# Optimization experiments

Hardware: AMD Instinct MI355X
Metric: run time of the kernel (lower is better)

Reference implementation:

```python
import jax, jax.numpy as jnp
import numpy as np

ACT_BITS = 8
NUM_HEADS = 6


def weight_quant(w):
    # BitNet b1.58 absmean ternary quantization with straight-through estimator
    scale = 1.0 / jnp.maximum(jnp.mean(jnp.abs(w)), 1e-5)
    wq = jnp.clip(jnp.round(w * scale), -1.0, 1.0) / scale
    return w + jax.lax.stop_gradient(wq - w)


def act_quant(x, bits=ACT_BITS):
    # per-token absmax quantization to `bits` bits, STE
    qb = float(2 ** (bits - 1))
    scale = qb / jnp.maximum(jnp.max(jnp.abs(x), axis=-1, keepdims=True), 1e-5)
    xq = jnp.clip(jnp.round(x * scale), -qb, qb - 1.0) / scale
    return x + jax.lax.stop_gradient(xq - x)


def bitlinear(x, w, b):
    return jnp.einsum('bnc,oc->bno', act_quant(x), weight_quant(w)) + b


def setup_inputs() -> dict:
    key = jax.random.key(0)
    ks = jax.random.split(key, 5)
    B, N, C = 8, 2048, 384
    return {
        'x': jax.random.normal(ks[0], (B, N, C), dtype=jnp.float32),
        'qkv_w': jax.random.normal(ks[1], (3 * C, C), dtype=jnp.float32) * 0.02,
        'qkv_b': jax.random.normal(ks[2], (3 * C,), dtype=jnp.float32) * 0.02,
        'proj_w': jax.random.normal(ks[3], (C, C), dtype=jnp.float32) * 0.02,
        'proj_b': jax.random.normal(ks[4], (C,), dtype=jnp.float32) * 0.02,
    }


def reference(x, qkv_w, qkv_b, proj_w, proj_b):
    B, N, C = x.shape
    H = NUM_HEADS
    D = C // H
    scale = D ** -0.5
    qkv = bitlinear(x, qkv_w, qkv_b)            # [B, N, 3C]
    q, k, v = jnp.split(qkv, 3, axis=-1)
    # [B, H, N, D]
    q = q.reshape(B, N, H, D).transpose(0, 2, 1, 3)
    k = k.reshape(B, N, H, D).transpose(0, 2, 1, 3)
    v = v.reshape(B, N, H, D).transpose(0, 2, 1, 3)
    # full [B, H, N, N] scores in float32, as in the original
    attn = jnp.einsum('bhnd,bhmd->bhnm', q.astype(jnp.float32), k.astype(jnp.float32)) * scale
    attn = jax.nn.softmax(attn, axis=-1).astype(q.dtype)
    out = jnp.einsum('bhnm,bhmd->bhnd', attn, v)
    out = out.transpose(0, 2, 1, 3).reshape(B, N, C)
    return bitlinear(out, proj_w, proj_b)
```

## Files before the change

### kernel.cpp

```cpp
#include <hip/hip_runtime.h>
#include <hip/hip_bf16.h>

typedef short  s16x8  __attribute__((ext_vector_type(8)));
typedef int    i32x4  __attribute__((ext_vector_type(4)));
typedef float  f32x16 __attribute__((ext_vector_type(16)));
typedef unsigned int u32x4 __attribute__((ext_vector_type(4)));
using u32 = unsigned int;
using u16 = unsigned short;
using as3u = __attribute__((address_space(3))) unsigned int;
using as1u = __attribute__((address_space(1))) unsigned int;

#define FINF __builtin_inff()

constexpr int B_  = 8;
constexpr int N_  = 2048;
constexpr int C_  = 384;
constexpr int H_  = 6;
constexpr int D_  = 64;
constexpr int BN_ = B_ * N_;
constexpr int O3_ = 3 * C_;
constexpr int NW1 = O3_ * C_;
constexpr int NW2 = C_ * C_;
constexpr int BH_ = B_ * H_;
constexpr int SPL = 2;

__device__ __forceinline__ u16 f2bf(float f) {
    union { float f; u32 u; } v; v.f = f;
    u32 r = v.u + 0x7FFFu + ((v.u >> 16) & 1u);
    return (u16)(r >> 16);
}
__device__ __forceinline__ float exp2a(float x) {
    float r; asm("v_exp_f32 %0, %1" : "=v"(r) : "v"(x)); return r;
}
__device__ __forceinline__ u32 cvtpk(float lo, float hi) {
    u32 r; asm("v_cvt_pk_bf16_f32 %0, %1, %2" : "=v"(r) : "v"(lo), "v"(hi)); return r;
}
__device__ __forceinline__ void plswap(u32& a, u32& b) {
    asm("v_permlane32_swap_b32 %0, %1" : "+v"(a), "+v"(b));
}
__device__ __forceinline__ float max3f(float a, float b, float c) {
    float r; asm("v_max3_f32 %0, %1, %2, %3" : "=v"(r) : "v"(a), "v"(b), "v"(c)); return r;
}
__device__ __forceinline__ u32 pack4i8(float a, float b, float c, float d) {
    int ia = (int)a, ib = (int)b, ic = (int)c, id = (int)d;
    return (u32)(ia & 255) | ((u32)(ib & 255) << 8) | ((u32)(ic & 255) << 16) | ((u32)(id & 255) << 24);
}

__global__ void k_wstats(const float* __restrict__ w1, const float* __restrict__ w2,
                         double* __restrict__ partial) {
    double s1 = 0.0, s2 = 0.0;
    int t = blockIdx.x * 256 + threadIdx.x;
    const int stride = 256 * 256;
    for (int i = t; i < NW1; i += stride) s1 += (double)fabsf(w1[i]);
    for (int i = t; i < NW2; i += stride) s2 += (double)fabsf(w2[i]);
#pragma unroll
    for (int m = 1; m < 64; m <<= 1) { s1 += __shfl_xor(s1, m, 64); s2 += __shfl_xor(s2, m, 64); }
    __shared__ double r1[4], r2[4];
    int wid = threadIdx.x >> 6;
    if ((threadIdx.x & 63) == 0) { r1[wid] = s1; r2[wid] = s2; }
    __syncthreads();
    if (threadIdx.x == 0) {
        partial[2 * blockIdx.x]     = r1[0] + r1[1] + r1[2] + r1[3];
        partial[2 * blockIdx.x + 1] = r2[0] + r2[1] + r2[2] + r2[3];
    }
}

__global__ void k_wfinal(const double* __restrict__ partial, float* __restrict__ scales) {
    int t = threadIdx.x;
    double s1 = partial[2 * t], s2 = partial[2 * t + 1];
#pragma unroll
    for (int m = 1; m < 64; m <<= 1) { s1 += __shfl_xor(s1, m, 64); s2 += __shfl_xor(s2, m, 64); }
    __shared__ double r1[4], r2[4];
    if ((t & 63) == 0) { r1[t >> 6] = s1; r2[t >> 6] = s2; }
    __syncthreads();
    if (t == 0) {
        float m1 = (float)((r1[0] + r1[1] + r1[2] + r1[3]) / (double)NW1);
        float m2 = (float)((r2[0] + r2[1] + r2[2] + r2[3]) / (double)NW2);
        float sc1 = 1.f / fmaxf(m1, 1e-5f);
        float sc2 = 1.f / fmaxf(m2, 1e-5f);
        scales[0] = sc1; scales[1] = 1.f / sc1;
        scales[2] = sc2; scales[3] = 1.f / sc2;
    }
}

__global__ void k_wquant(const float* __restrict__ w1, const float* __restrict__ w2,
                         const float* __restrict__ scales,
                         char* __restrict__ o1, char* __restrict__ o2) {
    float sc1 = scales[0], sc2 = scales[2];
    int t = blockIdx.x * blockDim.x + threadIdx.x;
    int stride = gridDim.x * blockDim.x;
    for (int i = t; i < NW1; i += stride)
        o1[i] = (char)(int)fminf(fmaxf(rintf(w1[i] * sc1), -1.f), 1.f);
    for (int i = t; i < NW2; i += stride)
        o2[i] = (char)(int)fminf(fmaxf(rintf(w2[i] * sc2), -1.f), 1.f);
}

__global__ __launch_bounds__(128) void k_aquant(const float* __restrict__ in,
                                                char* __restrict__ outq,
                                                float* __restrict__ rs) {
    int row = blockIdx.x;
    const float* xr = in + (size_t)row * C_;
    int t = threadIdx.x;
    float4 v = make_float4(0.f, 0.f, 0.f, 0.f);
    if (t < 96) v = ((const float4*)xr)[t];
    float mx = fmaxf(fmaxf(fabsf(v.x), fabsf(v.y)), fmaxf(fabsf(v.z), fabsf(v.w)));
#pragma unroll
    for (int m = 1; m < 64; m <<= 1) mx = fmaxf(mx, __shfl_xor(mx, m, 64));
    __shared__ float red[2];
    if ((t & 63) == 0) red[t >> 6] = mx;
    __syncthreads();
    mx = fmaxf(red[0], red[1]);
    float scale = 128.f / fmaxf(mx, 1e-5f);
    if (t == 0) rs[row] = 1.f / scale;
    if (t < 96) {
        float a = fminf(fmaxf(rintf(v.x * scale), -128.f), 127.f);
        float b = fminf(fmaxf(rintf(v.y * scale), -128.f), 127.f);
        float c = fminf(fmaxf(rintf(v.z * scale), -128.f), 127.f);
        float d = fminf(fmaxf(rintf(v.w * scale), -128.f), 127.f);
        ((u32*)(outq + (size_t)row * C_))[t] = pack4i8(a, b, c, d);
    }
}

template <int MODE>
__global__ __launch_bounds__(256) void k_gemm(const char* __restrict__ A, const char* __restrict__ W,
                                              const float* __restrict__ rs, const float* __restrict__ scales,
                                              const float* __restrict__ bias,
                                              u16* __restrict__ qg, u16* __restrict__ kg, u16* __restrict__ vtg,
                                              float* __restrict__ fout) {
    constexpr int K = C_;
    __shared__ char As[128 * 128];
    __shared__ char Bs[128 * 128];
    int m0 = blockIdx.x * 128, n0 = blockIdx.y * 128;
    int tid = threadIdx.x, lane = tid & 63, wid = tid >> 6;
    int wm = wid >> 1, wn = wid & 1;

    i32x4 acc[4][4];
#pragma unroll
    for (int a = 0; a < 4; ++a)
#pragma unroll
        for (int b = 0; b < 4; ++b)
#pragma unroll
            for (int r = 0; r < 4; ++r) acc[a][b][r] = 0;

    for (int k0 = 0; k0 < K; k0 += 128) {
#pragma unroll
        for (int t = 0; t < 4; ++t) {
            int P = t * 256 + wid * 64 + lane;
            int row = P >> 3, c8 = (P & 7) ^ (row & 7);
            const char* srcA = A + (size_t)(m0 + row) * K + k0 + c8 * 16;
            const char* srcB = W + (size_t)(n0 + row) * K + k0 + c8 * 16;
            __builtin_amdgcn_global_load_lds((const as1u*)srcA, (as3u*)(As + (size_t)(t * 256 + wid * 64) * 16), 16, 0, 0);
            __builtin_amdgcn_global_load_lds((const as1u*)srcB, (as3u*)(Bs + (size_t)(t * 256 + wid * 64) * 16), 16, 0, 0);
        }
        __syncthreads();
#pragma unroll
        for (int kk = 0; kk < 2; ++kk) {
            i32x4 ar[4], br[4];
#pragma unroll
            for (int f = 0; f < 4; ++f) {
                int rowA = wm * 64 + f * 16 + (lane & 15);
                int rowB = wn * 64 + f * 16 + (lane & 15);
                int cc = kk * 4 + (lane >> 4);
                ar[f] = *(const i32x4*)(&As[(size_t)(rowA * 8 + (cc ^ (rowA & 7))) * 16]);
                br[f] = *(const i32x4*)(&Bs[(size_t)(rowB * 8 + (cc ^ (rowB & 7))) * 16]);
            }
#pragma unroll
            for (int fr = 0; fr < 4; ++fr)
#pragma unroll
                for (int fc = 0; fc < 4; ++fc)
                    acc[fr][fc] = __builtin_amdgcn_mfma_i32_16x16x64_i8(ar[fr], br[fc], acc[fr][fc], 0, 0, 0);
        }
        __syncthreads();
    }

    float rsw = scales[MODE == 0 ? 1 : 3];
    int colg = lane & 15, rowb = (lane >> 4) * 4;
#pragma unroll
    for (int fr = 0; fr < 4; ++fr) {
#pragma unroll
        for (int r = 0; r < 4; ++r) {
            int m = m0 + wm * 64 + fr * 16 + rowb + r;
            float rsm = rs[m] * rsw;
#pragma unroll
            for (int fc = 0; fc < 4; ++fc) {
                int o = n0 + wn * 64 + fc * 16 + colg;
                float val = (float)acc[fr][fc][r] * rsm + bias[o];
                if (MODE == 0) {
                    int b = m >> 11, n = m & 2047;
                    if (o < C_) {
                        int hh = o >> 6, d = o & 63;
                        qg[(size_t)(b * H_ + hh) * (N_ * D_) + n * 64 + d] = f2bf(val * (0.125f * 1.44269504088896f));
                    } else if (o < 2 * C_) {
                        int oo = o - C_; int hh = oo >> 6, d = oo & 63;
                        kg[(size_t)(b * H_ + hh) * (N_ * D_) + n * 64 + d] = f2bf(val);
                    } else {
                        int oo = o - 2 * C_; int hh = oo >> 6, d = oo & 63;
                        vtg[(size_t)(b * H_ + hh) * (N_ * D_) + (size_t)d * N_ + n] = f2bf(val);
                    }
                } else {
                    fout[(size_t)m * C_ + o] = val;
                }
            }
        }
    }
}

__global__ __launch_bounds__(256, 4) void k_flash(const u16* __restrict__ qg, const u16* __restrict__ kg,
                                                  const u16* __restrict__ vtg,
                                                  float* __restrict__ pod, float* __restrict__ pml) {
    int i = blockIdx.x;
    int bh = (i & 7) * 6 + ((i >> 3) % 6);
    int x  = (i >> 3) / 6;
    int qt = x & 15;
    int split = x >> 4;
    int tid = threadIdx.x;
    int lane = tid & 63;
    int wid = tid >> 6;
    int h = lane >> 5;
    int ql = lane & 31;
    const u16* Qb = qg + (size_t)bh * (N_ * D_);
    const u16* Kb = kg + (size_t)bh * (N_ * D_);
    const u16* Vb = vtg + (size_t)bh * (N_ * D_);
    int q0 = qt * 128 + wid * 32;
    int kv_beg = split * (N_ / SPL);
    constexpr int NT = (N_ / SPL) / 64;

    __shared__ u16 Ks[2][64 * 64];
    __shared__ u16 Vs[2][64 * 64];

    s16x8 qf[4];
#pragma unroll
    for (int cs = 0; cs < 4; ++cs)
        qf[cs] = *(const s16x8*)(Qb + (size_t)(q0 + ql) * 64 + cs * 16 + h * 8);

    f32x16 od[2];
#pragma unroll
    for (int a = 0; a < 2; ++a)
#pragma unroll
        for (int r = 0; r < 16; ++r) od[a][r] = 0.f;

    float mrun = -FINF;
    float lrun = 0.f;

    auto STAGE = [&](int buf, int t0) {
        int kv0 = kv_beg + t0 * 64;
#pragma unroll
        for (int ii = 0; ii < 2; ++ii) {
            int P = (wid * 2 + ii) * 64 + lane;
            int row = P >> 3, c = (P & 7) ^ (row & 7);
            const u16* srcK = Kb + (size_t)(kv0 + row) * 64 + c * 8;
            __builtin_amdgcn_global_load_lds((const as1u*)srcK,
                (as3u*)(&Ks[buf][(size_t)(wid * 2 + ii) * 64 * 8]), 16, 0, 0);
            const u16* srcV = Vb + (size_t)row * N_ + kv0 + c * 8;
            __builtin_amdgcn_global_load_lds((const as1u*)srcV,
                (as3u*)(&Vs[buf][(size_t)(wid * 2 + ii) * 64 * 8]), 16, 0, 0);
        }
    };

    auto COMPUTE = [&](int buf) {
        f32x16 sA, sB;
#pragma unroll
        for (int r = 0; r < 16; ++r) { sA[r] = 0.f; sB[r] = 0.f; }
        __builtin_amdgcn_s_setprio(1);
#pragma unroll
        for (int cs = 0; cs < 4; ++cs) {
            int slot = (cs * 2 + h) ^ (ql & 7);
            s16x8 kf0 = *(const s16x8*)(&Ks[buf][(size_t)(ql * 8 + slot) * 8]);
            s16x8 kf1 = *(const s16x8*)(&Ks[buf][(size_t)((32 + ql) * 8 + slot) * 8]);
            sA = __builtin_amdgcn_mfma_f32_32x32x16_bf16(kf0, qf[cs], sA, 0, 0, 0);
            sB = __builtin_amdgcn_mfma_f32_32x32x16_bf16(kf1, qf[cs], sB, 0, 0, 0);
        }
        __builtin_amdgcn_s_setprio(0);

        float g0 = max3f(sA[0], sA[1], sA[2]),    g1 = max3f(sA[3], sA[4], sA[5]);
        float g2 = max3f(sA[6], sA[7], sA[8]),    g3 = max3f(sA[9], sA[10], sA[11]);
        float g4 = max3f(sA[12], sA[13], sA[14]), g5 = max3f(sA[15], sB[0], sB[1]);
        float g6 = max3f(sB[2], sB[3], sB[4]),    g7 = max3f(sB[5], sB[6], sB[7]);
        float g8 = max3f(sB[8], sB[9], sB[10]),   g9 = max3f(sB[11], sB[12], sB[13]);
        float g10 = fmaxf(sB[14], sB[15]);
        float h0 = max3f(g0, g1, g2), h1 = max3f(g3, g4, g5), h2 = max3f(g6, g7, g8);
        float mx = fmaxf(max3f(h0, h1, h2), fmaxf(g9, g10));
        mx = fmaxf(mx, __shfl_xor(mx, 32, 64));
        if (!__all(mx <= mrun + 8.f)) {
            float mnew = fmaxf(mrun, mx);
            float fsc = exp2a(mrun - mnew);
            lrun *= fsc;
#pragma unroll
            for (int r = 0; r < 16; ++r) { od[0][r] *= fsc; od[1][r] *= fsc; }
            mrun = mnew;
        }
        float m = mrun;
        float ps0 = 0.f, ps1 = 0.f, ps2 = 0.f, ps3 = 0.f;
#pragma unroll
        for (int r = 0; r < 16; r += 4) {
            float a0 = exp2a(sA[r] - m);     float a1 = exp2a(sA[r + 1] - m);
            float a2 = exp2a(sA[r + 2] - m); float a3 = exp2a(sA[r + 3] - m);
            float b0 = exp2a(sB[r] - m);     float b1 = exp2a(sB[r + 1] - m);
            float b2 = exp2a(sB[r + 2] - m); float b3 = exp2a(sB[r + 3] - m);
            sA[r] = a0; sA[r + 1] = a1; sA[r + 2] = a2; sA[r + 3] = a3;
            sB[r] = b0; sB[r + 1] = b1; sB[r + 2] = b2; sB[r + 3] = b3;
            ps0 += a0 + b0; ps1 += a1 + b1; ps2 += a2 + b2; ps3 += a3 + b3;
        }
        lrun += (ps0 + ps1) + (ps2 + ps3);

#pragma unroll
        for (int sl = 0; sl < 4; ++sl) {
            const int bse = (sl & 1) * 8;
            float p0, p1, p2, p3, p4, p5, p6, p7;
            if (sl < 2) {
                p0 = sA[bse + 0]; p1 = sA[bse + 1]; p2 = sA[bse + 2]; p3 = sA[bse + 3];
                p4 = sA[bse + 4]; p5 = sA[bse + 5]; p6 = sA[bse + 6]; p7 = sA[bse + 7];
            } else {
                p0 = sB[bse + 0]; p1 = sB[bse + 1]; p2 = sB[bse + 2]; p3 = sB[bse + 3];
                p4 = sB[bse + 4]; p5 = sB[bse + 5]; p6 = sB[bse + 6]; p7 = sB[bse + 7];
            }
            u32 A0 = cvtpk(p0, p1);
            u32 A1 = cvtpk(p2, p3);
            u32 B0 = cvtpk(p4, p5);
            u32 B1 = cvtpk(p6, p7);
            plswap(A0, B0);
            plswap(A1, B1);
            u32x4 pw; pw[0] = A0; pw[1] = A1; pw[2] = B0; pw[3] = B1;
            s16x8 pf = __builtin_bit_cast(s16x8, pw);
            __builtin_amdgcn_s_setprio(1);
#pragma unroll
            for (int db = 0; db < 2; ++db) {
                int vrow = db * 32 + ql;
                int slot = (sl * 2 + h) ^ (vrow & 7);
                s16x8 vf = *(const s16x8*)(&Vs[buf][(size_t)(vrow * 8 + slot) * 8]);
                od[db] = __builtin_amdgcn_mfma_f32_32x32x16_bf16(vf, pf, od[db], 0, 0, 0);
            }
            __builtin_amdgcn_s_setprio(0);
        }
    };

    STAGE(0, 0);
    for (int t = 0; t < NT; ++t) {
        if (t + 1 < NT) {
            STAGE((t + 1) & 1, t + 1);
            asm volatile("s_waitcnt vmcnt(4)" ::: "memory");
        } else {
            asm volatile("s_waitcnt vmcnt(0)" ::: "memory");
        }
        __builtin_amdgcn_s_barrier();
        __builtin_amdgcn_sched_barrier(0);
        COMPUTE(t & 1);
        __builtin_amdgcn_sched_barrier(0);
        __builtin_amdgcn_s_barrier();
    }

    {
        float ltot = lrun + __shfl_xor(lrun, 32, 64);
        int q = q0 + ql;
        float* op = pod + ((size_t)(split * BH_ + bh) * N_ + q) * 64;
#pragma unroll
        for (int db = 0; db < 2; ++db)
#pragma unroll
            for (int r = 0; r < 16; ++r) {
                int d = db * 32 + (r & 3) + 8 * (r >> 2) + 4 * h;
                op[d] = od[db][r];
            }
        if (h == 0) {
            float* mlp = pml + ((size_t)(split * BH_ + bh) * N_ + q) * 2;
            mlp[0] = mrun; mlp[1] = ltot;
        }
    }
}

__global__ __launch_bounds__(128) void k_caq(const float* __restrict__ pod,
                                             const float* __restrict__ pml,
                                             char* __restrict__ outq,
                                             float* __restrict__ rs) {
    int row = blockIdx.x;
    int b = row >> 11, q = row & (N_ - 1);
    int t = threadIdx.x;
    float4 o = make_float4(0.f, 0.f, 0.f, 0.f);
    if (t < 96) {
        int head = t >> 4, d4 = t & 15;
        int bh = b * H_ + head;
        const float2* ml = (const float2*)pml;
        float2 ml0 = ml[(size_t)bh * N_ + q];
        float2 ml1 = ml[(size_t)(BH_ + bh) * N_ + q];
        float m = fmaxf(ml0.x, ml1.x);
        float w0 = exp2a(ml0.x - m), w1 = exp2a(ml1.x - m);
        float inv = 1.f / (w0 * ml0.y + w1 * ml1.y);
        float4 a = ((const float4*)(pod + ((size_t)bh * N_ + q) * 64))[d4];
        float4 c = ((const float4*)(pod + ((size_t)(BH_ + bh) * N_ + q) * 64))[d4];
        o.x = (a.x * w0 + c.x * w1) * inv;
        o.y = (a.y * w0 + c.y * w1) * inv;
        o.z = (a.z * w0 + c.z * w1) * inv;
        o.w = (a.w * w0 + c.w * w1) * inv;
    }
    float mx = fmaxf(fmaxf(fabsf(o.x), fabsf(o.y)), fmaxf(fabsf(o.z), fabsf(o.w)));
#pragma unroll
    for (int m = 1; m < 64; m <<= 1) mx = fmaxf(mx, __shfl_xor(mx, m, 64));
    __shared__ float red[2];
    if ((t & 63) == 0) red[t >> 6] = mx;
    __syncthreads();
    mx = fmaxf(red[0], red[1]);
    float scale = 128.f / fmaxf(mx, 1e-5f);
    if (t == 0) rs[row] = 1.f / scale;
    if (t < 96) {
        float a = fminf(fmaxf(rintf(o.x * scale), -128.f), 127.f);
        float b2 = fminf(fmaxf(rintf(o.y * scale), -128.f), 127.f);
        float c = fminf(fmaxf(rintf(o.z * scale), -128.f), 127.f);
        float d = fminf(fmaxf(rintf(o.w * scale), -128.f), 127.f);
        ((u32*)(outq + (size_t)row * C_))[t] = pack4i8(a, b2, c, d);
    }
}

extern "C" void kernel_launch(void* const* d_in, const int* in_sizes, int n_in,
                              void* d_out, int out_size, void* d_ws, size_t ws_size,
                              hipStream_t stream) {
    const float* x      = (const float*)d_in[0];
    const float* qkv_w  = (const float*)d_in[1];
    const float* qkv_b  = (const float*)d_in[2];
    const float* proj_w = (const float*)d_in[3];
    const float* proj_b = (const float*)d_in[4];
    float* out = (float*)d_out;

    char* ws = (char*)d_ws;
    size_t off = 0;
    auto alloc = [&](size_t bytes) { size_t p = off; off += (bytes + 255) & ~(size_t)255; return p; };
    double* partial = (double*)(ws + alloc(256 * 2 * sizeof(double)));
    float*  scales  = (float*)(ws + alloc(4 * sizeof(float)));
    char*   wq1     = (char*)(ws + alloc((size_t)NW1));
    char*   wq2     = (char*)(ws + alloc((size_t)NW2));
    char*   xq      = (char*)(ws + alloc((size_t)BN_ * C_));
    float*  rsx     = (float*)(ws + alloc((size_t)BN_ * 4));
    float*  rsa     = (float*)(ws + alloc((size_t)BN_ * 4));
    u16*    qg      = (u16*)(ws + alloc((size_t)BH_ * N_ * D_ * 2));
    u16*    kg      = (u16*)(ws + alloc((size_t)BH_ * N_ * D_ * 2));
    u16*    vtg     = (u16*)(ws + alloc((size_t)BH_ * N_ * D_ * 2));
    float*  pod     = (float*)(ws + alloc((size_t)SPL * BH_ * N_ * 64 * 4));
    float*  pml     = (float*)(ws + alloc((size_t)SPL * BH_ * N_ * 2 * 4));
    (void)ws_size; (void)in_sizes; (void)n_in; (void)out_size;

    k_wstats<<<256, 256, 0, stream>>>(qkv_w, proj_w, partial);
    k_wfinal<<<1, 256, 0, stream>>>(partial, scales);
    k_wquant<<<512, 256, 0, stream>>>(qkv_w, proj_w, scales, wq1, wq2);
    k_aquant<<<BN_, 128, 0, stream>>>(x, xq, rsx);
    k_gemm<0><<<dim3(BN_ / 128, O3_ / 128), 256, 0, stream>>>(xq, wq1, rsx, scales, qkv_b, qg, kg, vtg, nullptr);
    k_flash<<<SPL * BH_ * (N_ / 128), 256, 0, stream>>>(qg, kg, vtg, pod, pml);
    k_caq<<<BN_, 128, 0, stream>>>(pod, pml, xq, rsa);
    k_gemm<1><<<dim3(BN_ / 128, C_ / 128), 256, 0, stream>>>(xq, wq2, rsa, scales, proj_b, nullptr, nullptr, nullptr, out);
}
```

Before: 148.2 us.

## Drop flash split-KV and write normalized bf16 attention output directly

Removes the two-way KV split in the flash attention kernel. Each block now processes the full KV range, normalizes its output by the softmax sum, and stores bf16 directly in [B,N,C] layout. The combine+quantize kernel becomes a plain bf16 per-row absmax quantizer, which removes the fp32 partial-output traffic and the merge math. The cost is half as many flash blocks (768 instead of 1536), each with twice the serial work, which may lower occupancy and latency hiding on the GPU.

New measurement: 142.1 us. -4.1%, faster.

```diff
diff --git a/kernel.cpp b/kernel.cpp
--- a/kernel.cpp
+++ b/kernel.cpp
@@ -5,6 +5,7 @@
 typedef int    i32x4  __attribute__((ext_vector_type(4)));
 typedef float  f32x16 __attribute__((ext_vector_type(16)));
 typedef unsigned int u32x4 __attribute__((ext_vector_type(4)));
+typedef unsigned int u32x2 __attribute__((ext_vector_type(2)));
 using u32 = unsigned int;
 using u16 = unsigned short;
 using as3u = __attribute__((address_space(3))) unsigned int;
@@ -22,12 +23,14 @@
 constexpr int NW1 = O3_ * C_;
 constexpr int NW2 = C_ * C_;
 constexpr int BH_ = B_ * H_;
-constexpr int SPL = 2;
 
 __device__ __forceinline__ u16 f2bf(float f) {
     union { float f; u32 u; } v; v.f = f;
     u32 r = v.u + 0x7FFFu + ((v.u >> 16) & 1u);
     return (u16)(r >> 16);
+}
+__device__ __forceinline__ float bf2f(u16 u) {
+    union { u32 i; float f; } v; v.i = (u32)u << 16; return v.f;
 }
 __device__ __forceinline__ float exp2a(float x) {
     float r; asm("v_exp_f32 %0, %1" : "=v"(r) : "v"(x)); return r;
@@ -103,6 +106,35 @@
     int t = threadIdx.x;
     float4 v = make_float4(0.f, 0.f, 0.f, 0.f);
     if (t < 96) v = ((const float4*)xr)[t];
+    float mx = fmaxf(fmaxf(fabsf(v.x), fabsf(v.y)), fmaxf(fabsf(v.z), fabsf(v.w)));
+#pragma unroll
+    for (int m = 1; m < 64; m <<= 1) mx = fmaxf(mx, __shfl_xor(mx, m, 64));
+    __shared__ float red[2];
+    if ((t & 63) == 0) red[t >> 6] = mx;
+    __syncthreads();
+    mx = fmaxf(red[0], red[1]);
+    float scale = 128.f / fmaxf(mx, 1e-5f);
+    if (t == 0) rs[row] = 1.f / scale;
+    if (t < 96) {
+        float a = fminf(fmaxf(rintf(v.x * scale), -128.f), 127.f);
+        float b = fminf(fmaxf(rintf(v.y * scale), -128.f), 127.f);
+        float c = fminf(fmaxf(rintf(v.z * scale), -128.f), 127.f);
+        float d = fminf(fmaxf(rintf(v.w * scale), -128.f), 127.f);
+        ((u32*)(outq + (size_t)row * C_))[t] = pack4i8(a, b, c, d);
+    }
+}
+
+__global__ __launch_bounds__(128) void k_caq(const u16* __restrict__ in,
+                                             char* __restrict__ outq,
+                                             float* __restrict__ rs) {
+    int row = blockIdx.x;
+    const u16* xr = in + (size_t)row * C_;
+    int t = threadIdx.x;
+    float4 v = make_float4(0.f, 0.f, 0.f, 0.f);
+    if (t < 96) {
+        ushort4 u = ((const ushort4*)xr)[t];
+        v.x = bf2f(u.x); v.y = bf2f(u.y); v.z = bf2f(u.z); v.w = bf2f(u.w);
+    }
     float mx = fmaxf(fmaxf(fabsf(v.x), fabsf(v.y)), fmaxf(fabsf(v.z), fabsf(v.w)));
 #pragma unroll
     for (int m = 1; m < 64; m <<= 1) mx = fmaxf(mx, __shfl_xor(mx, m, 64));
@@ -207,12 +239,10 @@
 
 __global__ __launch_bounds__(256, 4) void k_flash(const u16* __restrict__ qg, const u16* __restrict__ kg,
                                                   const u16* __restrict__ vtg,
-                                                  float* __restrict__ pod, float* __restrict__ pml) {
+                                                  u16* __restrict__ attno) {
     int i = blockIdx.x;
     int bh = (i & 7) * 6 + ((i >> 3) % 6);
-    int x  = (i >> 3) / 6;
-    int qt = x & 15;
-    int split = x >> 4;
+    int qt = (i >> 3) / 6;
     int tid = threadIdx.x;
     int lane = tid & 63;
     int wid = tid >> 6;
@@ -222,8 +252,7 @@
     const u16* Kb = kg + (size_t)bh * (N_ * D_);
     const u16* Vb = vtg + (size_t)bh * (N_ * D_);
     int q0 = qt * 128 + wid * 32;
-    int kv_beg = split * (N_ / SPL);
-    constexpr int NT = (N_ / SPL) / 64;
+    constexpr int NT = N_ / 64;
 
     __shared__ u16 Ks[2][64 * 64];
     __shared__ u16 Vs[2][64 * 64];
@@ -243,7 +272,7 @@
     float lrun = 0.f;
 
     auto STAGE = [&](int buf, int t0) {
-        int kv0 = kv_beg + t0 * 64;
+        int kv0 = t0 * 64;
 #pragma unroll
         for (int ii = 0; ii < 2; ++ii) {
             int P = (wid * 2 + ii) * 64 + lane;
@@ -351,61 +380,20 @@
 
     {
         float ltot = lrun + __shfl_xor(lrun, 32, 64);
+        float inv = 1.f / ltot;
+        int bb = bh / H_, head = bh - bb * H_;
         int q = q0 + ql;
-        float* op = pod + ((size_t)(split * BH_ + bh) * N_ + q) * 64;
+        u16* op = attno + ((size_t)(bb * N_ + q)) * C_ + head * 64;
 #pragma unroll
         for (int db = 0; db < 2; ++db)
 #pragma unroll
-            for (int r = 0; r < 16; ++r) {
-                int d = db * 32 + (r & 3) + 8 * (r >> 2) + 4 * h;
-                op[d] = od[db][r];
+            for (int rg = 0; rg < 4; ++rg) {
+                int d = db * 32 + 8 * rg + 4 * h;
+                u32x2 w;
+                w[0] = cvtpk(od[db][rg * 4 + 0] * inv, od[db][rg * 4 + 1] * inv);
+                w[1] = cvtpk(od[db][rg * 4 + 2] * inv, od[db][rg * 4 + 3] * inv);
+                *(u32x2*)(op + d) = w;
             }
-        if (h == 0) {
-            float* mlp = pml + ((size_t)(split * BH_ + bh) * N_ + q) * 2;
-            mlp[0] = mrun; mlp[1] = ltot;
-        }
-    }
-}
-
-__global__ __launch_bounds__(128) void k_caq(const float* __restrict__ pod,
-                                             const float* __restrict__ pml,
-                                             char* __restrict__ outq,
-                                             float* __restrict__ rs) {
-    int row = blockIdx.x;
-    int b = row >> 11, q = row & (N_ - 1);
-    int t = threadIdx.x;
-    float4 o = make_float4(0.f, 0.f, 0.f, 0.f);
-    if (t < 96) {
-        int head = t >> 4, d4 = t & 15;
-        int bh = b * H_ + head;
-        const float2* ml = (const float2*)pml;
-        float2 ml0 = ml[(size_t)bh * N_ + q];
-        float2 ml1 = ml[(size_t)(BH_ + bh) * N_ + q];
-        float m = fmaxf(ml0.x, ml1.x);
-        float w0 = exp2a(ml0.x - m), w1 = exp2a(ml1.x - m);
-        float inv = 1.f / (w0 * ml0.y + w1 * ml1.y);
-        float4 a = ((const float4*)(pod + ((size_t)bh * N_ + q) * 64))[d4];
-        float4 c = ((const float4*)(pod + ((size_t)(BH_ + bh) * N_ + q) * 64))[d4];
-        o.x = (a.x * w0 + c.x * w1) * inv;
-        o.y = (a.y * w0 + c.y * w1) * inv;
-        o.z = (a.z * w0 + c.z * w1) * inv;
-        o.w = (a.w * w0 + c.w * w1) * inv;
-    }
-    float mx = fmaxf(fmaxf(fabsf(o.x), fabsf(o.y)), fmaxf(fabsf(o.z), fabsf(o.w)));
-#pragma unroll
-    for (int m = 1; m < 64; m <<= 1) mx = fmaxf(mx, __shfl_xor(mx, m, 64));
-    __shared__ float red[2];
-    if ((t & 63) == 0) red[t >> 6] = mx;
-    __syncthreads();
-    mx = fmaxf(red[0], red[1]);
-    float scale = 128.f / fmaxf(mx, 1e-5f);
-    if (t == 0) rs[row] = 1.f / scale;
-    if (t < 96) {
-        float a = fminf(fmaxf(rintf(o.x * scale), -128.f), 127.f);
-        float b2 = fminf(fmaxf(rintf(o.y * scale), -128.f), 127.f);
-        float c = fminf(fmaxf(rintf(o.z * scale), -128.f), 127.f);
-        float d = fminf(fmaxf(rintf(o.w * scale), -128.f), 127.f);
-        ((u32*)(outq + (size_t)row * C_))[t] = pack4i8(a, b2, c, d);
     }
 }
 
@@ -432,8 +420,7 @@
     u16*    qg      = (u16*)(ws + alloc((size_t)BH_ * N_ * D_ * 2));
     u16*    kg      = (u16*)(ws + alloc((size_t)BH_ * N_ * D_ * 2));
     u16*    vtg     = (u16*)(ws + alloc((size_t)BH_ * N_ * D_ * 2));
-    float*  pod     = (float*)(ws + alloc((size_t)SPL * BH_ * N_ * 64 * 4));
-    float*  pml     = (float*)(ws + alloc((size_t)SPL * BH_ * N_ * 2 * 4));
+    u16*    attno   = (u16*)(ws + alloc((size_t)BN_ * C_ * 2));
     (void)ws_size; (void)in_sizes; (void)n_in; (void)out_size;
 
     k_wstats<<<256, 256, 0, stream>>>(qkv_w, proj_w, partial);
@@ -441,7 +428,7 @@
     k_wquant<<<512, 256, 0, stream>>>(qkv_w, proj_w, scales, wq1, wq2);
     k_aquant<<<BN_, 128, 0, stream>>>(x, xq, rsx);
     k_gemm<0><<<dim3(BN_ / 128, O3_ / 128), 256, 0, stream>>>(xq, wq1, rsx, scales, qkv_b, qg, kg, vtg, nullptr);
-    k_flash<<<SPL * BH_ * (N_ / 128), 256, 0, stream>>>(qg, kg, vtg, pod, pml);
-    k_caq<<<BN_, 128, 0, stream>>>(pod, pml, xq, rsa);
+    k_flash<<<BH_ * (N_ / 128), 256, 0, stream>>>(qg, kg, vtg, attno);
+    k_caq<<<BN_, 128, 0, stream>>>(attno, xq, rsa);
     k_gemm<1><<<dim3(BN_ / 128, C_ / 128), 256, 0, stream>>>(xq, wq2, rsa, scales, proj_b, nullptr, nullptr, nullptr, out);
 }
```
